# Kernel tuning notes

Hardware: AMD Instinct MI355X
Metric: run time of the kernel (lower is better)

Reference implementation:

```python
import math
import jax, jax.numpy as jnp
import numpy as np

B, T, L = 4096, 1024, 6  # batch, seq_length (threads), num_layers


def setup_inputs() -> dict:
    key = jax.random.key(0)
    k1, k2 = jax.random.split(key)
    X = jax.random.uniform(k1, (B, T), jnp.float32, -1.0, 1.0)
    weights = jax.random.uniform(k2, (L * T,), jnp.float32, -math.pi / 4, math.pi / 4)
    return {"X": X, "weights": weights}


def _dft_matrix(T):
    # Unitary DFT: F[j,k] = exp(-2*pi*i*j*k/T) / sqrt(T)
    idx = jnp.arange(T)
    F = jnp.exp((-2j * jnp.pi / T) * jnp.outer(idx, idx)).astype(jnp.complex64)
    return F * np.float32(1.0 / math.sqrt(T))


def reference(X, weights):
    # Analytic phasor-circuit simulation, batched over samples (no Python per-sample loop).
    # State: one complex phasor per thread, z_k = exp(i*phi_k).
    # shift(i, theta): z_i *= exp(i*theta)
    # mix(i, i+1): 2x2 balanced mixer [[1,1],[1,-1]]/sqrt(2) on adjacent pairs
    # dft(): unitary DFT across all threads
    Bb, Tt = X.shape
    Ll = weights.shape[0] // Tt
    w = weights.reshape(Ll, Tt)
    F = _dft_matrix(Tt)
    inv_sqrt2 = np.float32(1.0 / math.sqrt(2.0))

    phases = jnp.arcsin(jnp.clip(X, -0.999, 0.999))  # data encoding shifts
    z = jnp.exp(1j * phases).astype(jnp.complex64)    # [B, T]
    for l in range(Ll):
        z = z * jnp.exp(1j * w[l]).astype(jnp.complex64)          # variational shifts
        zp = z.reshape(Bb, Tt // 2, 2)                             # pairwise mix
        a, b = zp[..., 0], zp[..., 1]
        z = (jnp.stack([a + b, a - b], axis=-1) * inv_sqrt2).reshape(Bb, Tt)
        z = z @ F                                                  # DFT stage
    out_phase = jnp.angle(z[:, 0])                                 # phase of thread 0
    return (jnp.sin(out_phase) + 1.0) / 2.0                        # P(real), [B]
```

## Files before the change

### kernel.cpp

```cpp
#include <hip/hip_runtime.h>
#include <math.h>

#define TLEN 1024

typedef int i32x2 __attribute__((ext_vector_type(2)));

__device__ __forceinline__ float2 cadd(float2 a, float2 b){ return make_float2(a.x+b.x, a.y+b.y); }
__device__ __forceinline__ float2 csub(float2 a, float2 b){ return make_float2(a.x-b.x, a.y-b.y); }
__device__ __forceinline__ float2 cmul(float2 a, float2 b){
    return make_float2(fmaf(a.x, b.x, -(a.y*b.y)), fmaf(a.x, b.y, a.y*b.x));
}
__device__ __forceinline__ float2 cmulnegi(float2 a){ return make_float2(a.y, -a.x); }
__device__ __forceinline__ float2 cmulposi(float2 a){ return make_float2(-a.y, a.x); }
__device__ __forceinline__ int bitrev6(int l){
    return ((l & 1) << 5) | ((l & 2) << 3) | ((l & 4) << 1)
         | ((l & 8) >> 1) | ((l & 16) >> 3) | ((l & 32) >> 5);
}

#define DPP_XOR1  0xB1
#define DPP_XOR2  0x4E
#define DPP_XOR8  0x128
#define SWZ_XOR4  0x101F
#define SWZ_XOR16 0x401F

template<int CTRL>
__device__ __forceinline__ float2 dpp2(float2 v){
    return make_float2(
        __int_as_float(__builtin_amdgcn_mov_dpp(__float_as_int(v.x), CTRL, 0xF, 0xF, false)),
        __int_as_float(__builtin_amdgcn_mov_dpp(__float_as_int(v.y), CTRL, 0xF, 0xF, false)));
}
template<int PAT>
__device__ __forceinline__ float2 swz2(float2 v){
    return make_float2(
        __int_as_float(__builtin_amdgcn_ds_swizzle(__float_as_int(v.x), PAT)),
        __int_as_float(__builtin_amdgcn_ds_swizzle(__float_as_int(v.y), PAT)));
}
__device__ __forceinline__ float p32f(float v, bool up){
#if __has_builtin(__builtin_amdgcn_permlane32_swap)
    i32x2 r = __builtin_amdgcn_permlane32_swap(__float_as_int(v), __float_as_int(v), false, false);
    return __int_as_float(up ? r[0] : r[1]);
#else
    int a = __float_as_int(v), b = __float_as_int(v);
    asm("v_permlane32_swap_b32 %0, %1" : "+v"(a), "+v"(b));
    return __int_as_float(up ? a : b);
#endif
}
__device__ __forceinline__ float2 p32_2(float2 v, bool up){
    return make_float2(p32f(v.x, up), p32f(v.y, up));
}

__device__ __forceinline__ void dft4(float2 x0, float2 x1, float2 x2, float2 x3,
                                     float2& y0, float2& y1, float2& y2, float2& y3){
    float2 t0 = cadd(x0, x2);
    float2 t1 = csub(x0, x2);
    float2 t2 = cadd(x1, x3);
    float2 t3 = csub(x1, x3);
    float2 n3 = cmulnegi(t3);
    y0 = cadd(t0, t2);
    y2 = csub(t0, t2);
    y1 = cadd(t1, n3);
    y3 = csub(t1, n3);
}

__device__ __forceinline__ float2 combine4(float2 x0, float2 x1, float2 x2, float2 x3, int k){
    float2 e = cadd(x0, x2), f = csub(x0, x2);
    float2 g = cadd(x1, x3), h = csub(x1, x3);
    if (k == 0) return cadd(e, g);
    if (k == 1) return cadd(f, cmulnegi(h));
    if (k == 2) return csub(e, g);
    return cadd(f, cmulposi(h));
}

__device__ __forceinline__ void tw16(float2 u[4], int e){
    const float C1 = 0.92387953251128675613f, S1 = 0.38268343236508977173f;
    const float H  = 0.70710678118654752440f;
    if (e == 1){
        u[1] = cmul(u[1], make_float2( C1, -S1));
        u[2] = cmul(u[2], make_float2(  H,  -H));
        u[3] = cmul(u[3], make_float2( S1, -C1));
    } else if (e == 2){
        u[1] = cmul(u[1], make_float2(  H,  -H));
        u[2] = cmulnegi(u[2]);
        u[3] = cmul(u[3], make_float2( -H,  -H));
    } else if (e == 3){
        u[1] = cmul(u[1], make_float2( S1, -C1));
        u[2] = cmul(u[2], make_float2( -H,  -H));
        u[3] = cmul(u[3], make_float2(-C1,  S1));
    }
}

template<bool TW, typename F>
__device__ __forceinline__ void dif_stage4(float2 z[4], F partner, float sg, float2 w){
    #pragma unroll
    for (int r = 0; r < 4; ++r){
        float2 o = partner(z[r]);
        float2 pre = make_float2(fmaf(sg, z[r].x, o.x), fmaf(sg, z[r].y, o.y));
        z[r] = TW ? cmul(pre, w) : pre;
    }
}
template<bool TW, typename F>
__device__ __forceinline__ void dit_stage4(float2 z[4], F partner, float sg, float2 w){
    #pragma unroll
    for (int r = 0; r < 4; ++r){
        float2 zz = TW ? cmul(z[r], w) : z[r];
        float2 o = partner(zz);
        z[r] = make_float2(fmaf(sg, zz.x, o.x), fmaf(sg, zz.y, o.y));
    }
}
__device__ __forceinline__ void xfft_dif4(float2 z[4], const float2 Wt[5], int lane){
    const float2 ONE = make_float2(1.0f, 0.0f);
    {   const bool up = (lane & 32) != 0; const float sg = up ? -1.0f : 1.0f;
        dif_stage4<true>(z, [&](float2 v){ return p32_2(v, up); }, sg, up ? Wt[4] : ONE); }
    {   const bool up = (lane & 16) != 0; const float sg = up ? -1.0f : 1.0f;
        dif_stage4<true>(z, [](float2 v){ return swz2<SWZ_XOR16>(v); }, sg, up ? Wt[3] : ONE); }
    {   const bool up = (lane & 8) != 0;  const float sg = up ? -1.0f : 1.0f;
        dif_stage4<true>(z, [](float2 v){ return dpp2<DPP_XOR8>(v); }, sg, up ? Wt[2] : ONE); }
    {   const bool up = (lane & 4) != 0;  const float sg = up ? -1.0f : 1.0f;
        dif_stage4<true>(z, [](float2 v){ return swz2<SWZ_XOR4>(v); }, sg, up ? Wt[1] : ONE); }
    {   const bool up = (lane & 2) != 0;  const float sg = up ? -1.0f : 1.0f;
        dif_stage4<true>(z, [](float2 v){ return dpp2<DPP_XOR2>(v); }, sg, up ? Wt[0] : ONE); }
    {   const float sg = (lane & 1) ? -1.0f : 1.0f;
        dif_stage4<false>(z, [](float2 v){ return dpp2<DPP_XOR1>(v); }, sg, ONE); }
}
__device__ __forceinline__ void xfft_dit4(float2 z[4], const float2 Wt[5], int lane){
    const float2 ONE = make_float2(1.0f, 0.0f);
    {   const float sg = (lane & 1) ? -1.0f : 1.0f;
        dit_stage4<false>(z, [](float2 v){ return dpp2<DPP_XOR1>(v); }, sg, ONE); }
    {   const bool up = (lane & 2) != 0;  const float sg = up ? -1.0f : 1.0f;
        dit_stage4<true>(z, [](float2 v){ return dpp2<DPP_XOR2>(v); }, sg, up ? Wt[0] : ONE); }
    {   const bool up = (lane & 4) != 0;  const float sg = up ? -1.0f : 1.0f;
        dit_stage4<true>(z, [](float2 v){ return swz2<SWZ_XOR4>(v); }, sg, up ? Wt[1] : ONE); }
    {   const bool up = (lane & 8) != 0;  const float sg = up ? -1.0f : 1.0f;
        dit_stage4<true>(z, [](float2 v){ return dpp2<DPP_XOR8>(v); }, sg, up ? Wt[2] : ONE); }
    {   const bool up = (lane & 16) != 0; const float sg = up ? -1.0f : 1.0f;
        dit_stage4<true>(z, [](float2 v){ return swz2<SWZ_XOR16>(v); }, sg, up ? Wt[3] : ONE); }
    {   const bool up = (lane & 32) != 0; const float sg = up ? -1.0f : 1.0f;
        dit_stage4<true>(z, [&](float2 v){ return p32_2(v, up); }, sg, up ? Wt[4] : ONE); }
}

__global__ __launch_bounds__(512, 4)
void fused_kernel(const float* __restrict__ X,
                  const float* __restrict__ W,
                  float* __restrict__ out)
{
    __shared__ float2 xb0[16 * 64];
    __shared__ float2 xb1[16 * 64];

    const int lane = threadIdx.x & 63;
    const int wid  = threadIdx.x >> 6;
    const int row  = blockIdx.x * 8 + wid;

    float4 xr[4];
    {
        const float4* px = (const float4*)(X + (size_t)row * TLEN + lane * 16);
        #pragma unroll
        for (int i = 0; i < 4; ++i) xr[i] = px[i];
    }

    if (wid < 4){
        const int c = bitrev6(lane);
        float2 Wt[5];
        #pragma unroll
        for (int k = 0; k < 5; ++k){
            const int h = 2 << k;
            float sv, cv;
            __sincosf(-3.14159265358979323846f * (float)(lane & (h - 1)) / (float)h, &sv, &cv);
            Wt[k] = make_float2(cv, sv);
        }
        float2 wmv[4];
        {
            const float theta = -6.28318530717958647692f * (float)c / 1024.0f;
            float sv, cv;
            __sincosf(theta * (float)(4 * wid), &sv, &cv); float2 base = make_float2(cv, sv);
            __sincosf(theta, &sv, &cv);                    float2 step = make_float2(cv, sv);
            wmv[0] = base;
            wmv[1] = cmul(wmv[0], step);
            wmv[2] = cmul(wmv[1], step);
            wmv[3] = cmul(wmv[2], step);
        }

        float2 z[4];
        #pragma unroll
        for (int j = 0; j < 4; ++j) z[j] = make_float2(1.0f, 0.0f);

        auto Mstr = [&](){
            const bool upm = (lane & 32) != 0;
            const float sgm = upm ? -1.0f : 1.0f;
            #pragma unroll
            for (int j = 0; j < 4; ++j){
                float2 o = p32_2(z[j], upm);
                z[j] = make_float2(fmaf(sgm, z[j].x, o.x), fmaf(sgm, z[j].y, o.y));
            }
        };
        auto Mcon = [&](){
            float2 a0 = z[0], b0 = z[1], a1 = z[2], b1 = z[3];
            z[0] = cadd(a0, b0); z[1] = csub(a0, b0);
            z[2] = cadd(a1, b1); z[3] = csub(a1, b1);
        };
        auto Dstr = [&](int l){
            const float* p = W + l * TLEN + c + 64 * wid;
            #pragma unroll
            for (int j = 0; j < 4; ++j){
                float sv, cv; __sincosf(p[j << 8], &sv, &cv);
                z[j] = cmul(z[j], make_float2(cv, sv));
            }
        };
        auto Dcon = [&](int l){
            float4 wv = *(const float4*)(W + l * TLEN + 16 * lane + 4 * wid);
            float ws[4] = {wv.x, wv.y, wv.z, wv.w};
            #pragma unroll
            for (int j = 0; j < 4; ++j){
                float sv, cv; __sincosf(ws[j], &sv, &cv);
                z[j] = cmul(z[j], make_float2(cv, sv));
            }
        };
        auto midtw = [&](){
            #pragma unroll
            for (int j = 0; j < 4; ++j) z[j] = cmul(z[j], wmv[j]);
        };
        auto fft16A = [&](){
            #pragma unroll
            for (int j = 0; j < 4; ++j) xb1[(wid * 4 + j) * 64 + lane] = z[j];
            __syncthreads();
            float2 u[4];
            #pragma unroll
            for (int j = 0; j < 4; ++j){
                float2 x0 = xb1[(0 * 4 + j) * 64 + lane];
                float2 x1 = xb1[(1 * 4 + j) * 64 + lane];
                float2 x2 = xb1[(2 * 4 + j) * 64 + lane];
                float2 x3 = xb1[(3 * 4 + j) * 64 + lane];
                u[j] = combine4(x0, x1, x2, x3, wid);
            }
            tw16(u, wid);
            dft4(u[0], u[1], u[2], u[3], z[0], z[1], z[2], z[3]);
        };
        auto fft16B = [&](){
            float2 u[4];
            dft4(z[0], z[1], z[2], z[3], u[0], u[1], u[2], u[3]);
            tw16(u, wid);
            #pragma unroll
            for (int j = 0; j < 4; ++j) xb0[(wid * 4 + j) * 64 + lane] = u[j];
            __syncthreads();
            #pragma unroll
            for (int j = 0; j < 4; ++j){
                float2 x0 = xb0[(0 * 4 + j) * 64 + lane];
                float2 x1 = xb0[(1 * 4 + j) * 64 + lane];
                float2 x2 = xb0[(2 * 4 + j) * 64 + lane];
                float2 x3 = xb0[(3 * 4 + j) * 64 + lane];
                z[j] = combine4(x0, x1, x2, x3, wid);
            }
        };
        auto dftA = [&](){ xfft_dif4(z, Wt, lane); midtw(); fft16A(); };
        auto dftB = [&](){ fft16B(); midtw(); xfft_dit4(z, Wt, lane); };

        Mstr(); Dstr(5);
        #pragma unroll 1
        for (int lp = 0; lp < 2; ++lp){
            dftB(); Mcon(); Dcon(4 - 2 * lp);
            dftA(); Mstr(); Dstr(3 - 2 * lp);
        }
        dftB(); Mcon(); Dcon(0);
        #pragma unroll
        for (int j = 0; j < 4; ++j) xb1[(4 * wid + j) * 64 + lane] = z[j];
        __syncthreads();
    } else {
        #pragma unroll 1
        for (int i = 0; i < 6; ++i) __syncthreads();
    }

    float re = 0.0f, im = 0.0f;
    #pragma unroll
    for (int i = 0; i < 4; ++i){
        float4 xv = xr[i];
        float xs[4] = {xv.x, xv.y, xv.z, xv.w};
        #pragma unroll
        for (int j = 0; j < 4; ++j){
            float2 av = xb1[(4 * i + j) * 64 + lane];
            float x  = fminf(fmaxf(xs[j], -0.999f), 0.999f);
            float cc = sqrtf(fmaf(-x, x, 1.0f));
            re = fmaf(av.x, cc, re);  re = fmaf(-av.y, x,  re);
            im = fmaf(av.x, x,  im);  im = fmaf( av.y, cc, im);
        }
    }

    float2 s = make_float2(re, im);
    s = cadd(s, dpp2<DPP_XOR1>(s));
    s = cadd(s, dpp2<DPP_XOR2>(s));
    s = cadd(s, swz2<SWZ_XOR4>(s));
    s = cadd(s, dpp2<DPP_XOR8>(s));
    s = cadd(s, swz2<SWZ_XOR16>(s));
    s = cadd(s, p32_2(s, (lane & 32) != 0));

    if (lane == 0){
        out[row] = fmaf(s.y * rsqrtf(fmaf(s.x, s.x, s.y * s.y)), 0.5f, 0.5f);
    }
}

extern "C" void kernel_launch(void* const* d_in, const int* in_sizes, int n_in,
                              void* d_out, int out_size, void* d_ws, size_t ws_size,
                              hipStream_t stream) {
    const float* X = (const float*)d_in[0];
    const float* W = (const float*)d_in[1];
    float* out = (float*)d_out;
    (void)in_sizes; (void)n_in; (void)out_size; (void)d_ws; (void)ws_size;

    fused_kernel<<<4096 / 8, 512, 0, stream>>>(X, W, out);
}
```

Measured before the change: 18.01 us.

## Precompute weight sincos tables in LDS using idle waves

The four otherwise idle waves of each block now compute cos/sin of the weights for layers 0 to 4 and store them as complex tables in shared memory. The layout is permuted so the compute waves can read them directly in their layouts. The compute waves replace their per-layer __sincosf calls with LDS loads, taking transcendental work off their critical path. In exchange, shared memory per block grows by about 40KB, which may limit resident blocks. Correctness relies on the first barrier inside dftB ordering the table writes before the first table use.

```diff
diff --git a/kernel.cpp b/kernel.cpp
--- a/kernel.cpp
+++ b/kernel.cpp
@@ -143,6 +143,8 @@
                   const float* __restrict__ W,
                   float* __restrict__ out)
 {
+    __shared__ float2 tblE[3 * TLEN];
+    __shared__ float2 tblO[2 * TLEN];
     __shared__ float2 xb0[16 * 64];
     __shared__ float2 xb1[16 * 64];
 
@@ -197,7 +199,7 @@
             z[0] = cadd(a0, b0); z[1] = csub(a0, b0);
             z[2] = cadd(a1, b1); z[3] = csub(a1, b1);
         };
-        auto Dstr = [&](int l){
+        auto DstrSin = [&](int l){
             const float* p = W + l * TLEN + c + 64 * wid;
             #pragma unroll
             for (int j = 0; j < 4; ++j){
@@ -205,14 +207,15 @@
                 z[j] = cmul(z[j], make_float2(cv, sv));
             }
         };
+        auto Dstr = [&](int l){
+            const float2* p = tblO + ((l - 1) >> 1) * TLEN + 64 * wid + c;
+            #pragma unroll
+            for (int j = 0; j < 4; ++j) z[j] = cmul(z[j], p[j << 8]);
+        };
         auto Dcon = [&](int l){
-            float4 wv = *(const float4*)(W + l * TLEN + 16 * lane + 4 * wid);
-            float ws[4] = {wv.x, wv.y, wv.z, wv.w};
-            #pragma unroll
-            for (int j = 0; j < 4; ++j){
-                float sv, cv; __sincosf(ws[j], &sv, &cv);
-                z[j] = cmul(z[j], make_float2(cv, sv));
-            }
+            const float2* p = tblE + (l >> 1) * TLEN + (4 * wid) * 64 + lane;
+            #pragma unroll
+            for (int j = 0; j < 4; ++j) z[j] = cmul(z[j], p[j << 6]);
         };
         auto midtw = [&](){
             #pragma unroll
@@ -253,7 +256,7 @@
         auto dftA = [&](){ xfft_dif4(z, Wt, lane); midtw(); fft16A(); };
         auto dftB = [&](){ fft16B(); midtw(); xfft_dit4(z, Wt, lane); };
 
-        Mstr(); Dstr(5);
+        Mstr(); DstrSin(5);
         #pragma unroll 1
         for (int lp = 0; lp < 2; ++lp){
             dftB(); Mcon(); Dcon(4 - 2 * lp);
@@ -264,8 +267,21 @@
         for (int j = 0; j < 4; ++j) xb1[(4 * wid + j) * 64 + lane] = z[j];
         __syncthreads();
     } else {
+        const int pt = threadIdx.x - 256;
         #pragma unroll 1
-        for (int i = 0; i < 6; ++i) __syncthreads();
+        for (int i = pt; i < 3 * TLEN; i += 256){
+            int le = i >> 10, t = i & 1023;
+            float sv, cv; __sincosf(W[2 * le * TLEN + t], &sv, &cv);
+            tblE[le * TLEN + ((t & 15) << 6) + (t >> 4)] = make_float2(cv, sv);
+        }
+        #pragma unroll 1
+        for (int i = pt; i < 2 * TLEN; i += 256){
+            int lo = i >> 10, t = i & 1023;
+            float sv, cv; __sincosf(W[(2 * lo + 1) * TLEN + t], &sv, &cv);
+            tblO[i] = make_float2(cv, sv);
+        }
+        #pragma unroll 1
+        for (int b = 0; b < 6; ++b) __syncthreads();
     }
 
     float re = 0.0f, im = 0.0f;
```

Measured after the change: 21.10 us. 1.17x slower.

## Spread weight-circuit FFT across all eight waves with two elements per lane

Applied to the files above, without the earlier changes.

The weight-only phasor circuit was computed by four waves holding four complex values per lane while the other four waves only hit barriers. Now all eight waves take part, each lane holding two values. The size-16 cross-wave FFT is reorganised into a radix-8 combine read from shared memory plus one radix-2 butterfly in registers, with new twiddle and index layouts. This halves per-lane serial cross-lane shuffle and sincos work, at the cost of more shared-memory reads per combine step.

```diff
diff --git a/kernel.cpp b/kernel.cpp
--- a/kernel.cpp
+++ b/kernel.cpp
@@ -49,19 +49,6 @@
     return make_float2(p32f(v.x, up), p32f(v.y, up));
 }
 
-__device__ __forceinline__ void dft4(float2 x0, float2 x1, float2 x2, float2 x3,
-                                     float2& y0, float2& y1, float2& y2, float2& y3){
-    float2 t0 = cadd(x0, x2);
-    float2 t1 = csub(x0, x2);
-    float2 t2 = cadd(x1, x3);
-    float2 t3 = csub(x1, x3);
-    float2 n3 = cmulnegi(t3);
-    y0 = cadd(t0, t2);
-    y2 = csub(t0, t2);
-    y1 = cadd(t1, n3);
-    y3 = csub(t1, n3);
-}
-
 __device__ __forceinline__ float2 combine4(float2 x0, float2 x1, float2 x2, float2 x3, int k){
     float2 e = cadd(x0, x2), f = csub(x0, x2);
     float2 g = cadd(x1, x3), h = csub(x1, x3);
@@ -70,72 +57,67 @@
     if (k == 2) return csub(e, g);
     return cadd(f, cmulposi(h));
 }
-
-__device__ __forceinline__ void tw16(float2 u[4], int e){
-    const float C1 = 0.92387953251128675613f, S1 = 0.38268343236508977173f;
-    const float H  = 0.70710678118654752440f;
-    if (e == 1){
-        u[1] = cmul(u[1], make_float2( C1, -S1));
-        u[2] = cmul(u[2], make_float2(  H,  -H));
-        u[3] = cmul(u[3], make_float2( S1, -C1));
-    } else if (e == 2){
-        u[1] = cmul(u[1], make_float2(  H,  -H));
-        u[2] = cmulnegi(u[2]);
-        u[3] = cmul(u[3], make_float2( -H,  -H));
-    } else if (e == 3){
-        u[1] = cmul(u[1], make_float2( S1, -C1));
-        u[2] = cmul(u[2], make_float2( -H,  -H));
-        u[3] = cmul(u[3], make_float2(-C1,  S1));
-    }
+__device__ __forceinline__ float2 combine8(const float2 x[8], int k){
+    const float H = 0.70710678118654752440f;
+    float2 E = combine4(x[0], x[2], x[4], x[6], k & 3);
+    float2 O = combine4(x[1], x[3], x[5], x[7], k & 3);
+    float2 WO;
+    switch (k & 3){
+        case 0:  WO = O; break;
+        case 1:  WO = cmul(O, make_float2( H, -H)); break;
+        case 2:  WO = cmulnegi(O); break;
+        default: WO = cmul(O, make_float2(-H, -H)); break;
+    }
+    return (k < 4) ? cadd(E, WO) : csub(E, WO);
 }
 
 template<bool TW, typename F>
-__device__ __forceinline__ void dif_stage4(float2 z[4], F partner, float sg, float2 w){
-    #pragma unroll
-    for (int r = 0; r < 4; ++r){
+__device__ __forceinline__ void dif_stage2(float2 z[2], F partner, float sg, float2 w){
+    #pragma unroll
+    for (int r = 0; r < 2; ++r){
         float2 o = partner(z[r]);
         float2 pre = make_float2(fmaf(sg, z[r].x, o.x), fmaf(sg, z[r].y, o.y));
         z[r] = TW ? cmul(pre, w) : pre;
     }
 }
 template<bool TW, typename F>
-__device__ __forceinline__ void dit_stage4(float2 z[4], F partner, float sg, float2 w){
-    #pragma unroll
-    for (int r = 0; r < 4; ++r){
+__device__ __forceinline__ void dit_stage2(float2 z[2], F partner, float sg, float2 w){
+    #pragma unroll
+    for (int r = 0; r < 2; ++r){
         float2 zz = TW ? cmul(z[r], w) : z[r];
         float2 o = partner(zz);
         z[r] = make_float2(fmaf(sg, zz.x, o.x), fmaf(sg, zz.y, o.y));
     }
 }
-__device__ __forceinline__ void xfft_dif4(float2 z[4], const float2 Wt[5], int lane){
+__device__ __forceinline__ void xfft_dif2(float2 z[2], const float2 Wt[5], int lane){
     const float2 ONE = make_float2(1.0f, 0.0f);
     {   const bool up = (lane & 32) != 0; const float sg = up ? -1.0f : 1.0f;
-        dif_stage4<true>(z, [&](float2 v){ return p32_2(v, up); }, sg, up ? Wt[4] : ONE); }
+        dif_stage2<true>(z, [&](float2 v){ return p32_2(v, up); }, sg, up ? Wt[4] : ONE); }
     {   const bool up = (lane & 16) != 0; const float sg = up ? -1.0f : 1.0f;
-        dif_stage4<true>(z, [](float2 v){ return swz2<SWZ_XOR16>(v); }, sg, up ? Wt[3] : ONE); }
+        dif_stage2<true>(z, [](float2 v){ return swz2<SWZ_XOR16>(v); }, sg, up ? Wt[3] : ONE); }
     {   const bool up = (lane & 8) != 0;  const float sg = up ? -1.0f : 1.0f;
-        dif_stage4<true>(z, [](float2 v){ return dpp2<DPP_XOR8>(v); }, sg, up ? Wt[2] : ONE); }
+        dif_stage2<true>(z, [](float2 v){ return dpp2<DPP_XOR8>(v); }, sg, up ? Wt[2] : ONE); }
     {   const bool up = (lane & 4) != 0;  const float sg = up ? -1.0f : 1.0f;
-        dif_stage4<true>(z, [](float2 v){ return swz2<SWZ_XOR4>(v); }, sg, up ? Wt[1] : ONE); }
+        dif_stage2<true>(z, [](float2 v){ return swz2<SWZ_XOR4>(v); }, sg, up ? Wt[1] : ONE); }
     {   const bool up = (lane & 2) != 0;  const float sg = up ? -1.0f : 1.0f;
-        dif_stage4<true>(z, [](float2 v){ return dpp2<DPP_XOR2>(v); }, sg, up ? Wt[0] : ONE); }
+        dif_stage2<true>(z, [](float2 v){ return dpp2<DPP_XOR2>(v); }, sg, up ? Wt[0] : ONE); }
     {   const float sg = (lane & 1) ? -1.0f : 1.0f;
-        dif_stage4<false>(z, [](float2 v){ return dpp2<DPP_XOR1>(v); }, sg, ONE); }
-}
-__device__ __forceinline__ void xfft_dit4(float2 z[4], const float2 Wt[5], int lane){
+        dif_stage2<false>(z, [](float2 v){ return dpp2<DPP_XOR1>(v); }, sg, ONE); }
+}
+__device__ __forceinline__ void xfft_dit2(float2 z[2], const float2 Wt[5], int lane){
     const float2 ONE = make_float2(1.0f, 0.0f);
     {   const float sg = (lane & 1) ? -1.0f : 1.0f;
-        dit_stage4<false>(z, [](float2 v){ return dpp2<DPP_XOR1>(v); }, sg, ONE); }
+        dit_stage2<false>(z, [](float2 v){ return dpp2<DPP_XOR1>(v); }, sg, ONE); }
     {   const bool up = (lane & 2) != 0;  const float sg = up ? -1.0f : 1.0f;
-        dit_stage4<true>(z, [](float2 v){ return dpp2<DPP_XOR2>(v); }, sg, up ? Wt[0] : ONE); }
+        dit_stage2<true>(z, [](float2 v){ return dpp2<DPP_XOR2>(v); }, sg, up ? Wt[0] : ONE); }
     {   const bool up = (lane & 4) != 0;  const float sg = up ? -1.0f : 1.0f;
-        dit_stage4<true>(z, [](float2 v){ return swz2<SWZ_XOR4>(v); }, sg, up ? Wt[1] : ONE); }
+        dit_stage2<true>(z, [](float2 v){ return swz2<SWZ_XOR4>(v); }, sg, up ? Wt[1] : ONE); }
     {   const bool up = (lane & 8) != 0;  const float sg = up ? -1.0f : 1.0f;
-        dit_stage4<true>(z, [](float2 v){ return dpp2<DPP_XOR8>(v); }, sg, up ? Wt[2] : ONE); }
+        dit_stage2<true>(z, [](float2 v){ return dpp2<DPP_XOR8>(v); }, sg, up ? Wt[2] : ONE); }
     {   const bool up = (lane & 16) != 0; const float sg = up ? -1.0f : 1.0f;
-        dit_stage4<true>(z, [](float2 v){ return swz2<SWZ_XOR16>(v); }, sg, up ? Wt[3] : ONE); }
+        dit_stage2<true>(z, [](float2 v){ return swz2<SWZ_XOR16>(v); }, sg, up ? Wt[3] : ONE); }
     {   const bool up = (lane & 32) != 0; const float sg = up ? -1.0f : 1.0f;
-        dit_stage4<true>(z, [&](float2 v){ return p32_2(v, up); }, sg, up ? Wt[4] : ONE); }
+        dit_stage2<true>(z, [&](float2 v){ return p32_2(v, up); }, sg, up ? Wt[4] : ONE); }
 }
 
 __global__ __launch_bounds__(512, 4)
@@ -157,116 +139,112 @@
         for (int i = 0; i < 4; ++i) xr[i] = px[i];
     }
 
-    if (wid < 4){
-        const int c = bitrev6(lane);
-        float2 Wt[5];
-        #pragma unroll
-        for (int k = 0; k < 5; ++k){
-            const int h = 2 << k;
-            float sv, cv;
-            __sincosf(-3.14159265358979323846f * (float)(lane & (h - 1)) / (float)h, &sv, &cv);
-            Wt[k] = make_float2(cv, sv);
-        }
-        float2 wmv[4];
-        {
-            const float theta = -6.28318530717958647692f * (float)c / 1024.0f;
-            float sv, cv;
-            __sincosf(theta * (float)(4 * wid), &sv, &cv); float2 base = make_float2(cv, sv);
-            __sincosf(theta, &sv, &cv);                    float2 step = make_float2(cv, sv);
-            wmv[0] = base;
-            wmv[1] = cmul(wmv[0], step);
-            wmv[2] = cmul(wmv[1], step);
-            wmv[3] = cmul(wmv[2], step);
-        }
-
-        float2 z[4];
-        #pragma unroll
-        for (int j = 0; j < 4; ++j) z[j] = make_float2(1.0f, 0.0f);
-
-        auto Mstr = [&](){
-            const bool upm = (lane & 32) != 0;
-            const float sgm = upm ? -1.0f : 1.0f;
+    const int c = bitrev6(lane);
+    float2 Wt[5];
+    #pragma unroll
+    for (int k = 0; k < 5; ++k){
+        const int h = 2 << k;
+        float sv, cv;
+        __sincosf(-3.14159265358979323846f * (float)(lane & (h - 1)) / (float)h, &sv, &cv);
+        Wt[k] = make_float2(cv, sv);
+    }
+    float2 w16;
+    {
+        float sv, cv;
+        __sincosf(-3.14159265358979323846f * (float)wid / 8.0f, &sv, &cv);
+        w16 = make_float2(cv, sv);
+    }
+    float2 wmv[2];
+    {
+        const float theta = -6.28318530717958647692f * (float)c / 1024.0f;
+        float sv, cv;
+        __sincosf(theta * (float)(2 * wid), &sv, &cv); wmv[0] = make_float2(cv, sv);
+        __sincosf(theta, &sv, &cv);                    wmv[1] = cmul(wmv[0], make_float2(cv, sv));
+    }
+
+    float2 z[2];
+    z[0] = make_float2(1.0f, 0.0f);
+    z[1] = make_float2(1.0f, 0.0f);
+
+    auto Mstr = [&](){
+        const bool upm = (lane & 32) != 0;
+        const float sgm = upm ? -1.0f : 1.0f;
+        #pragma unroll
+        for (int j = 0; j < 2; ++j){
+            float2 o = p32_2(z[j], upm);
+            z[j] = make_float2(fmaf(sgm, z[j].x, o.x), fmaf(sgm, z[j].y, o.y));
+        }
+    };
+    auto Mcon = [&](){
+        float2 a0 = z[0], b0 = z[1];
+        z[0] = cadd(a0, b0); z[1] = csub(a0, b0);
+    };
+    auto Dstr = [&](int l){
+        const float* p = W + l * TLEN + c + 64 * wid;
+        #pragma unroll
+        for (int j = 0; j < 2; ++j){
+            float sv, cv; __sincosf(p[j << 9], &sv, &cv);
+            z[j] = cmul(z[j], make_float2(cv, sv));
+        }
+    };
+    auto Dcon = [&](int l){
+        float2 wv = *(const float2*)(W + l * TLEN + 16 * lane + 2 * wid);
+        float ws[2] = {wv.x, wv.y};
+        #pragma unroll
+        for (int j = 0; j < 2; ++j){
+            float sv, cv; __sincosf(ws[j], &sv, &cv);
+            z[j] = cmul(z[j], make_float2(cv, sv));
+        }
+    };
+    auto midtw = [&](){
+        z[0] = cmul(z[0], wmv[0]);
+        z[1] = cmul(z[1], wmv[1]);
+    };
+    auto fft16A = [&](){
+        #pragma unroll
+        for (int j = 0; j < 2; ++j) xb1[(wid * 2 + j) * 64 + lane] = z[j];
+        __syncthreads();
+        float2 u[2];
+        #pragma unroll
+        for (int j = 0; j < 2; ++j){
+            float2 x[8];
             #pragma unroll
-            for (int j = 0; j < 4; ++j){
-                float2 o = p32_2(z[j], upm);
-                z[j] = make_float2(fmaf(sgm, z[j].x, o.x), fmaf(sgm, z[j].y, o.y));
-            }
-        };
-        auto Mcon = [&](){
-            float2 a0 = z[0], b0 = z[1], a1 = z[2], b1 = z[3];
-            z[0] = cadd(a0, b0); z[1] = csub(a0, b0);
-            z[2] = cadd(a1, b1); z[3] = csub(a1, b1);
-        };
-        auto Dstr = [&](int l){
-            const float* p = W + l * TLEN + c + 64 * wid;
+            for (int w = 0; w < 8; ++w) x[w] = xb1[(2 * w + j) * 64 + lane];
+            u[j] = combine8(x, wid);
+        }
+        u[1] = cmul(u[1], w16);
+        z[0] = cadd(u[0], u[1]);
+        z[1] = csub(u[0], u[1]);
+    };
+    auto fft16B = [&](){
+        float2 u[2];
+        u[0] = cadd(z[0], z[1]);
+        u[1] = csub(z[0], z[1]);
+        u[1] = cmul(u[1], w16);
+        #pragma unroll
+        for (int j = 0; j < 2; ++j) xb0[(wid * 2 + j) * 64 + lane] = u[j];
+        __syncthreads();
+        #pragma unroll
+        for (int j = 0; j < 2; ++j){
+            float2 x[8];
             #pragma unroll
-            for (int j = 0; j < 4; ++j){
-                float sv, cv; __sincosf(p[j << 8], &sv, &cv);
-                z[j] = cmul(z[j], make_float2(cv, sv));
-            }
-        };
-        auto Dcon = [&](int l){
-            float4 wv = *(const float4*)(W + l * TLEN + 16 * lane + 4 * wid);
-            float ws[4] = {wv.x, wv.y, wv.z, wv.w};
-            #pragma unroll
-            for (int j = 0; j < 4; ++j){
-                float sv, cv; __sincosf(ws[j], &sv, &cv);
-                z[j] = cmul(z[j], make_float2(cv, sv));
-            }
-        };
-        auto midtw = [&](){
-            #pragma unroll
-            for (int j = 0; j < 4; ++j) z[j] = cmul(z[j], wmv[j]);
-        };
-        auto fft16A = [&](){
-            #pragma unroll
-            for (int j = 0; j < 4; ++j) xb1[(wid * 4 + j) * 64 + lane] = z[j];
-            __syncthreads();
-            float2 u[4];
-            #pragma unroll
-            for (int j = 0; j < 4; ++j){
-                float2 x0 = xb1[(0 * 4 + j) * 64 + lane];
-                float2 x1 = xb1[(1 * 4 + j) * 64 + lane];
-                float2 x2 = xb1[(2 * 4 + j) * 64 + lane];
-                float2 x3 = xb1[(3 * 4 + j) * 64 + lane];
-                u[j] = combine4(x0, x1, x2, x3, wid);
-            }
-            tw16(u, wid);
-            dft4(u[0], u[1], u[2], u[3], z[0], z[1], z[2], z[3]);
-        };
-        auto fft16B = [&](){
-            float2 u[4];
-            dft4(z[0], z[1], z[2], z[3], u[0], u[1], u[2], u[3]);
-            tw16(u, wid);
-            #pragma unroll
-            for (int j = 0; j < 4; ++j) xb0[(wid * 4 + j) * 64 + lane] = u[j];
-            __syncthreads();
-            #pragma unroll
-            for (int j = 0; j < 4; ++j){
-                float2 x0 = xb0[(0 * 4 + j) * 64 + lane];
-                float2 x1 = xb0[(1 * 4 + j) * 64 + lane];
-                float2 x2 = xb0[(2 * 4 + j) * 64 + lane];
-                float2 x3 = xb0[(3 * 4 + j) * 64 + lane];
-                z[j] = combine4(x0, x1, x2, x3, wid);
-            }
-        };
-        auto dftA = [&](){ xfft_dif4(z, Wt, lane); midtw(); fft16A(); };
-        auto dftB = [&](){ fft16B(); midtw(); xfft_dit4(z, Wt, lane); };
-
-        Mstr(); Dstr(5);
-        #pragma unroll 1
-        for (int lp = 0; lp < 2; ++lp){
-            dftB(); Mcon(); Dcon(4 - 2 * lp);
-            dftA(); Mstr(); Dstr(3 - 2 * lp);
-        }
-        dftB(); Mcon(); Dcon(0);
-        #pragma unroll
-        for (int j = 0; j < 4; ++j) xb1[(4 * wid + j) * 64 + lane] = z[j];
-        __syncthreads();
-    } else {
-        #pragma unroll 1
-        for (int i = 0; i < 6; ++i) __syncthreads();
-    }
+            for (int w = 0; w < 8; ++w) x[w] = xb0[(2 * w + j) * 64 + lane];
+            z[j] = combine8(x, wid);
+        }
+    };
+    auto dftA = [&](){ xfft_dif2(z, Wt, lane); midtw(); fft16A(); };
+    auto dftB = [&](){ fft16B(); midtw(); xfft_dit2(z, Wt, lane); };
+
+    Mstr(); Dstr(5);
+    #pragma unroll 1
+    for (int lp = 0; lp < 2; ++lp){
+        dftB(); Mcon(); Dcon(4 - 2 * lp);
+        dftA(); Mstr(); Dstr(3 - 2 * lp);
+    }
+    dftB(); Mcon(); Dcon(0);
+    #pragma unroll
+    for (int j = 0; j < 2; ++j) xb1[(2 * wid + j) * 64 + lane] = z[j];
+    __syncthreads();
 
     float re = 0.0f, im = 0.0f;
     #pragma unroll
```

Measured after the change: 17.47 us. 1.03x faster.
